# Kernel tuning notes

Hardware: AMD Instinct MI355X
Metric: run time of the kernel (lower is better)

The kernel has to match this reference:

```python
import math
import jax, jax.numpy as jnp
import numpy as np

NUM_HEADS = 16
HIDDEN = 1024
FILL = -10000000000000.0


def setup_inputs() -> dict:
    key = jax.random.key(0)
    ks = jax.random.split(key, 12)
    B, S, H = 4, 2048, HIDDEN
    scale = 1.0 / math.sqrt(H)
    inp = {
        "query": jax.random.normal(ks[0], (B, S, H), jnp.float32),
        "key": jax.random.normal(ks[1], (B, S, H), jnp.float32),
        "value": jax.random.normal(ks[2], (B, S, H), jnp.float32),
        "mask": jnp.ones((B, S), jnp.float32),
        # torch.nn.Linear weights are [out, in]; y = x @ W.T + b
        "Wq": jax.random.normal(ks[3], (H, H), jnp.float32) * scale,
        "bq": jax.random.normal(ks[4], (H,), jnp.float32) * 0.01,
        "Wk": jax.random.normal(ks[5], (H, H), jnp.float32) * scale,
        "bk": jax.random.normal(ks[6], (H,), jnp.float32) * 0.01,
        "Wv": jax.random.normal(ks[7], (H, H), jnp.float32) * scale,
        "bv": jax.random.normal(ks[8], (H,), jnp.float32) * 0.01,
        "Wo": jax.random.normal(ks[9], (H, H), jnp.float32) * scale,
        "bo": jax.random.normal(ks[10], (H,), jnp.float32) * 0.01,
    }
    return inp


def reference(query, key, value, mask, Wq, bq, Wk, bk, Wv, bv, Wo, bo):
    B, S, H = query.shape
    nh = NUM_HEADS
    dh = H // nh

    def proj(x, W, b):
        # [B,S,H] -> [B,nh,S,dh]
        y = x @ W.T + b
        return y.reshape(B, S, nh, dh).transpose(0, 2, 1, 3)

    q = proj(query, Wq, bq)
    k = proj(key, Wk, bk)
    v = proj(value, Wv, bv)

    # mask_tril=True: combined padding + causal mask [B,1,S,S]
    tril = jnp.tril(jnp.ones((S, S), query.dtype))
    m = jnp.einsum("bs,ls->bls", mask, tril)[:, None]

    scores = jnp.einsum("bhqd,bhkd->bhqk", q, k) / math.sqrt(dh)
    scores = jnp.where(m == 0, jnp.asarray(FILL, scores.dtype), scores)
    probs = jax.nn.softmax(scores, axis=-1)  # dropout p=0 -> identity

    out = jnp.einsum("bhqv,bhvd->bhqd", probs, v)
    out = out.transpose(0, 2, 1, 3).reshape(B, S, H)
    return out @ Wo.T + bo
```

## Files before the change

kernel.cpp:

```cpp
#include <hip/hip_runtime.h>
#include <hip/hip_bf16.h>
#include <math.h>

#define BATCH 4
#define SEQ   2048
#define HID   1024
#define NH    16
#define DH    64
#define MTOT  (BATCH * SEQ)
#define FILLV (-1e13f)

typedef unsigned short ushort_t;
typedef short bf16x8 __attribute__((ext_vector_type(8)));
typedef float f32x4  __attribute__((ext_vector_type(4)));

__device__ __forceinline__ float bf2f(ushort_t u) {
    return __uint_as_float(((unsigned int)u) << 16);
}
__device__ __forceinline__ ushort_t f2bf(float f) {
    union { __hip_bfloat16 h; ushort_t u; } cv;
    cv.h = __float2bfloat16(f);
    return cv.u;
}

__device__ __forceinline__ void gload16(const void* g, void* l) {
    __builtin_amdgcn_global_load_lds(
        (const __attribute__((address_space(1))) unsigned int*)g,
        (__attribute__((address_space(3))) unsigned int*)l, 16, 0, 0);
}

__global__ __launch_bounds__(256) void cast_f32_bf16(
    const float* __restrict__ x, ushort_t* __restrict__ y, int n4)
{
    const int i = blockIdx.x * 256 + threadIdx.x;
    if (i < n4) {
        const float4 v = ((const float4*)x)[i];
        ushort4 o;
        o.x = f2bf(v.x); o.y = f2bf(v.y); o.z = f2bf(v.z); o.w = f2bf(v.w);
        ((ushort4*)y)[i] = o;
    }
}

template <bool OUT_BF16, bool BIAS_ROW>
__global__ __launch_bounds__(256) void gemm_bt_mfma(
    const ushort_t* __restrict__ A,
    const ushort_t* __restrict__ W,
    const float*    __restrict__ bias,
    void* __restrict__ Yv,
    int M, int N, int K)
{
    __shared__ ushort_t As[2][4096];
    __shared__ ushort_t Bs[2][4096];

    const int tid  = threadIdx.x;
    const int lane = tid & 63;
    const int wave = tid >> 6;
    const int wm   = wave & 1;
    const int wn   = wave >> 1;

    const int flat = blockIdx.y * gridDim.x + blockIdx.x;
    const int cpx  = (gridDim.x * gridDim.y) >> 3;
    const int fl2  = (flat & 7) * cpx + (flat >> 3);
    const int bx   = fl2 % gridDim.x;
    const int by   = fl2 / gridDim.x;

    const int m0   = by * 128;
    const int n0   = bx * 128;
    const int lr   = lane & 15;
    const int lk   = (lane >> 4) * 8;

    f32x4 acc[4][4];
#pragma unroll
    for (int i = 0; i < 4; i++)
#pragma unroll
        for (int j = 0; j < 4; j++) acc[i][j] = (f32x4){0.f, 0.f, 0.f, 0.f};

    auto STAGE = [&](int kk, int d) {
        const ushort_t* a = A + (size_t)(m0 + wave * 32 + lr) * K + kk + lk;
        const ushort_t* w = W + (size_t)(n0 + wave * 32 + lr) * K + kk + lk;
        ushort_t* al = &As[d][wave * 1024];
        ushort_t* bl = &Bs[d][wave * 1024];
        gload16(a,                 al);
        gload16(a + (size_t)16 * K, al + 512);
        gload16(w,                 bl);
        gload16(w + (size_t)16 * K, bl + 512);
    };

    const int nk = K >> 5;
    STAGE(0, 0);

    for (int kt = 0; kt < nk; ++kt) {
        const int d = kt & 1;
        if (kt + 1 < nk) {
            STAGE((kt + 1) << 5, d ^ 1);
            asm volatile("s_waitcnt vmcnt(4)" ::: "memory");
        } else {
            asm volatile("s_waitcnt vmcnt(0)" ::: "memory");
        }
        __builtin_amdgcn_s_barrier();
        __builtin_amdgcn_sched_barrier(0);

        bf16x8 af[4], bf[4];
#pragma unroll
        for (int i = 0; i < 4; i++)
            af[i] = *(const bf16x8*)&As[d][(wm * 4 + i) * 512 + lane * 8];
#pragma unroll
        for (int j = 0; j < 4; j++)
            bf[j] = *(const bf16x8*)&Bs[d][(wn * 4 + j) * 512 + lane * 8];
#pragma unroll
        for (int i = 0; i < 4; i++)
#pragma unroll
            for (int j = 0; j < 4; j++)
                acc[i][j] = __builtin_amdgcn_mfma_f32_16x16x32_bf16(
                    af[i], bf[j], acc[i][j], 0, 0, 0);

        __builtin_amdgcn_sched_barrier(0);
        __builtin_amdgcn_s_barrier();
    }

    const int orow = (lane >> 4) * 4;
    const int ocol = lane & 15;

#pragma unroll
    for (int i = 0; i < 4; i++) {
#pragma unroll
        for (int j = 0; j < 4; j++) {
            const int col = n0 + wn * 64 + j * 16 + ocol;
#pragma unroll
            for (int r = 0; r < 4; r++) {
                const int row = m0 + wm * 64 + i * 16 + orow + r;
                const float bvv = BIAS_ROW ? bias[row] : bias[col];
                const float v = acc[i][j][r] + bvv;
                if (OUT_BF16)
                    ((ushort_t*)Yv)[(size_t)row * N + col] = f2bf(v);
                else
                    ((float*)Yv)[(size_t)row * N + col] = v;
            }
        }
    }
}

__global__ __launch_bounds__(256, 2) void attn_mfma(
    const ushort_t* __restrict__ Qp,
    const ushort_t* __restrict__ Kp,
    const ushort_t* __restrict__ Vt,
    const float*    __restrict__ mask,
    ushort_t* __restrict__ Op)
{
    __shared__ ushort_t Kl[2][4096];
    __shared__ ushort_t Vl[2][4096];
    __shared__ ushort_t PlA[4][16 * 72];
    __shared__ ushort_t PlB[4][16 * 72];

    const int tid  = threadIdx.x;
    const int lane = tid & 63;
    const int wave = tid >> 6;
    const int li   = lane & 15;
    const int lq   = lane >> 4;
    const int blk  = blockIdx.x;
    const int xcd = blk & 7;
    const int jj  = blk >> 3;
    const int bh  = xcd * 8 + (jj & 7);
    const int pp  = jj >> 3;
    const int pr  = pp * 4 + wave;
    const int h   = bh & (NH - 1);
    const int b   = bh >> 4;
    const int prow = lq * 4;

    const int q0a = pr * 16;
    const int q0b = (127 - pr) * 16;
    const int qrowA = q0a + li;
    const int qrowB = q0b + li;
    const int jmaxB = 31 - pp;

    const size_t bSEQ = (size_t)b * SEQ;
    const int    hoff = h * DH;

    const int srow = tid >> 3;
    const int scs8 = ((tid & 7) ^ (srow & 7)) * 8;

    const int fr0 = li * 64 + ((lq ^ (li & 7)) * 8);

    ushort_t* pwA = &PlA[wave][0];
    ushort_t* pwB = &PlB[wave][0];

    const float* mbase = mask + bSEQ + prow;

    const size_t qaA = (bSEQ + qrowA) * HID + hoff + lq * 8;
    const size_t qaB = (bSEQ + qrowB) * HID + hoff + lq * 8;
    const bf16x8 qfA0 = *(const bf16x8*)&Qp[qaA];
    const bf16x8 qfA1 = *(const bf16x8*)&Qp[qaA + 32];
    const bf16x8 qfB0 = *(const bf16x8*)&Qp[qaB];
    const bf16x8 qfB1 = *(const bf16x8*)&Qp[qaB + 32];

    f32x4 oaA[4], oaB[4];
#pragma unroll
    for (int nt = 0; nt < 4; nt++) {
        oaA[nt] = (f32x4){0.f, 0.f, 0.f, 0.f};
        oaB[nt] = (f32x4){0.f, 0.f, 0.f, 0.f};
    }
    float mA = -1e30f, lA = 0.f, mB = -1e30f, lB = 0.f;

    auto STAGE = [&](int js, int bs) {
        const size_t k0s = (size_t)js * 64;
        const ushort_t* kg = Kp + (bSEQ + k0s + srow) * HID + hoff + scs8;
        ushort_t* kl = &Kl[bs][wave * 512];
        gload16(kg, kl);
        gload16(kg + (size_t)32 * HID, kl + 2048);
        const ushort_t* vg = Vt + (size_t)(hoff + srow) * MTOT + bSEQ + k0s + scs8;
        ushort_t* vl = &Vl[bs][wave * 512];
        gload16(vg, vl);
        gload16(vg + (size_t)32 * MTOT, vl + 2048);
    };

    STAGE(0, 0);

    for (int j = 0; j <= jmaxB; ++j) {
        const int  k0  = j * 64;
        const int  bs  = j & 1;
        const bool doA = (j <= pp);

        f32x4 mk[4];
#pragma unroll
        for (int nt = 0; nt < 4; nt++)
            mk[nt] = *(const f32x4*)&mbase[k0 + nt * 16];
        __builtin_amdgcn_sched_barrier(0);

        const int jn = (j < jmaxB) ? (j + 1) : jmaxB;
        STAGE(jn, bs ^ 1);

        asm volatile("s_waitcnt vmcnt(8)" ::: "memory");
        __builtin_amdgcn_s_barrier();
        __builtin_amdgcn_sched_barrier(0);

        bf16x8 kf[4][2];
#pragma unroll
        for (int nt = 0; nt < 4; nt++) {
            const int eo = nt * 1024 + fr0;
            kf[nt][0] = *(const bf16x8*)&Kl[bs][eo];
            kf[nt][1] = *(const bf16x8*)&Kl[bs][eo ^ 32];
        }

        f32x4 saA[4], saB[4];
        __builtin_amdgcn_s_setprio(1);
#pragma unroll
        for (int nt = 0; nt < 4; nt++) {
            f32x4 a = (f32x4){0.f, 0.f, 0.f, 0.f};
            a = __builtin_amdgcn_mfma_f32_16x16x32_bf16(kf[nt][0], qfB0, a, 0, 0, 0);
            a = __builtin_amdgcn_mfma_f32_16x16x32_bf16(kf[nt][1], qfB1, a, 0, 0, 0);
            saB[nt] = a;
        }
        if (doA) {
#pragma unroll
            for (int nt = 0; nt < 4; nt++) {
                f32x4 a = (f32x4){0.f, 0.f, 0.f, 0.f};
                a = __builtin_amdgcn_mfma_f32_16x16x32_bf16(kf[nt][0], qfA0, a, 0, 0, 0);
                a = __builtin_amdgcn_mfma_f32_16x16x32_bf16(kf[nt][1], qfA1, a, 0, 0, 0);
                saA[nt] = a;
            }
        }
        __builtin_amdgcn_s_setprio(0);

        float sB[4][4];
#pragma unroll
        for (int nt = 0; nt < 4; nt++)
#pragma unroll
            for (int r = 0; r < 4; r++) {
                const float v = saB[nt][r] * 0.125f;
                sB[nt][r] = (mk[nt][r] == 0.f) ? FILLV : v;
            }
        if (k0 + 63 > q0b) {
#pragma unroll
            for (int nt = 0; nt < 4; nt++)
#pragma unroll
                for (int r = 0; r < 4; r++) {
                    const int kpos = k0 + nt * 16 + prow + r;
                    sB[nt][r] = (kpos > qrowB) ? FILLV : sB[nt][r];
                }
        }
        float pmB = fmaxf(fmaxf(sB[0][0], sB[0][1]), fmaxf(sB[0][2], sB[0][3]));
#pragma unroll
        for (int nt = 1; nt < 4; nt++)
            pmB = fmaxf(pmB, fmaxf(fmaxf(sB[nt][0], sB[nt][1]),
                                   fmaxf(sB[nt][2], sB[nt][3])));
        pmB = fmaxf(pmB, __shfl_xor(pmB, 16));
        pmB = fmaxf(pmB, __shfl_xor(pmB, 32));
        const float mnB = fmaxf(mB, pmB);
        const float alB = __expf(mB - mnB);
        mB = mnB;
        float psB = 0.f;
#pragma unroll
        for (int nt = 0; nt < 4; nt++) {
            const float p0 = __expf(sB[nt][0] - mnB);
            const float p1 = __expf(sB[nt][1] - mnB);
            const float p2 = __expf(sB[nt][2] - mnB);
            const float p3 = __expf(sB[nt][3] - mnB);
            psB += (p0 + p1) + (p2 + p3);
            ushort4 pk;
            pk.x = f2bf(p0); pk.y = f2bf(p1); pk.z = f2bf(p2); pk.w = f2bf(p3);
            *(ushort4*)&pwB[li * 72 + nt * 16 + prow] = pk;
        }
        psB += __shfl_xor(psB, 16);
        psB += __shfl_xor(psB, 32);
        lB = lB * alB + psB;

        float alA = 1.f;
        if (doA) {
            float sA[4][4];
#pragma unroll
            for (int nt = 0; nt < 4; nt++)
#pragma unroll
                for (int r = 0; r < 4; r++) {
                    const float v = saA[nt][r] * 0.125f;
                    sA[nt][r] = (mk[nt][r] == 0.f) ? FILLV : v;
                }
            if (k0 + 63 > q0a) {
#pragma unroll
                for (int nt = 0; nt < 4; nt++)
#pragma unroll
                    for (int r = 0; r < 4; r++) {
                        const int kpos = k0 + nt * 16 + prow + r;
                        sA[nt][r] = (kpos > qrowA) ? FILLV : sA[nt][r];
                    }
            }
            float pmA = fmaxf(fmaxf(sA[0][0], sA[0][1]), fmaxf(sA[0][2], sA[0][3]));
#pragma unroll
            for (int nt = 1; nt < 4; nt++)
                pmA = fmaxf(pmA, fmaxf(fmaxf(sA[nt][0], sA[nt][1]),
                                       fmaxf(sA[nt][2], sA[nt][3])));
            pmA = fmaxf(pmA, __shfl_xor(pmA, 16));
            pmA = fmaxf(pmA, __shfl_xor(pmA, 32));
            const float mnA = fmaxf(mA, pmA);
            alA = __expf(mA - mnA);
            mA = mnA;
            float psA = 0.f;
#pragma unroll
            for (int nt = 0; nt < 4; nt++) {
                const float p0 = __expf(sA[nt][0] - mnA);
                const float p1 = __expf(sA[nt][1] - mnA);
                const float p2 = __expf(sA[nt][2] - mnA);
                const float p3 = __expf(sA[nt][3] - mnA);
                psA += (p0 + p1) + (p2 + p3);
                ushort4 pk;
                pk.x = f2bf(p0); pk.y = f2bf(p1); pk.z = f2bf(p2); pk.w = f2bf(p3);
                *(ushort4*)&pwA[li * 72 + nt * 16 + prow] = pk;
            }
            psA += __shfl_xor(psA, 16);
            psA += __shfl_xor(psA, 32);
            lA = lA * alA + psA;
        }

        const bf16x8 pfB0 = *(const bf16x8*)&pwB[li * 72 + lq * 8];
        const bf16x8 pfB1 = *(const bf16x8*)&pwB[li * 72 + 32 + lq * 8];
        bf16x8 vf[4][2];
#pragma unroll
        for (int nt = 0; nt < 4; nt++) {
            const int eo = nt * 1024 + fr0;
            vf[nt][0] = *(const bf16x8*)&Vl[bs][eo];
            vf[nt][1] = *(const bf16x8*)&Vl[bs][eo ^ 32];
        }

        __builtin_amdgcn_s_setprio(1);
#pragma unroll
        for (int nt = 0; nt < 4; nt++) {
            f32x4 o = oaB[nt];
#pragma unroll
            for (int r = 0; r < 4; r++) o[r] *= alB;
            o = __builtin_amdgcn_mfma_f32_16x16x32_bf16(vf[nt][0], pfB0, o, 0, 0, 0);
            o = __builtin_amdgcn_mfma_f32_16x16x32_bf16(vf[nt][1], pfB1, o, 0, 0, 0);
            oaB[nt] = o;
        }
        __builtin_amdgcn_s_setprio(0);
        if (doA) {
            const bf16x8 pfA0 = *(const bf16x8*)&pwA[li * 72 + lq * 8];
            const bf16x8 pfA1 = *(const bf16x8*)&pwA[li * 72 + 32 + lq * 8];
            __builtin_amdgcn_s_setprio(1);
#pragma unroll
            for (int nt = 0; nt < 4; nt++) {
                f32x4 o = oaA[nt];
#pragma unroll
                for (int r = 0; r < 4; r++) o[r] *= alA;
                o = __builtin_amdgcn_mfma_f32_16x16x32_bf16(vf[nt][0], pfA0, o, 0, 0, 0);
                o = __builtin_amdgcn_mfma_f32_16x16x32_bf16(vf[nt][1], pfA1, o, 0, 0, 0);
                oaA[nt] = o;
            }
            __builtin_amdgcn_s_setprio(0);
        }

        __builtin_amdgcn_sched_barrier(0);
        __builtin_amdgcn_s_barrier();
    }
    asm volatile("s_waitcnt vmcnt(0)" ::: "memory");

    {
        const float linv = 1.f / lB;
        const size_t obase = (bSEQ + qrowB) * HID + hoff + prow;
#pragma unroll
        for (int nt = 0; nt < 4; nt++) {
            ushort4 ov;
            ov.x = f2bf(oaB[nt][0] * linv);
            ov.y = f2bf(oaB[nt][1] * linv);
            ov.z = f2bf(oaB[nt][2] * linv);
            ov.w = f2bf(oaB[nt][3] * linv);
            *(ushort4*)&Op[obase + nt * 16] = ov;
        }
    }
    {
        const float linv = 1.f / lA;
        const size_t obase = (bSEQ + qrowA) * HID + hoff + prow;
#pragma unroll
        for (int nt = 0; nt < 4; nt++) {
            ushort4 ov;
            ov.x = f2bf(oaA[nt][0] * linv);
            ov.y = f2bf(oaA[nt][1] * linv);
            ov.z = f2bf(oaA[nt][2] * linv);
            ov.w = f2bf(oaA[nt][3] * linv);
            *(ushort4*)&Op[obase + nt * 16] = ov;
        }
    }
}

extern "C" void kernel_launch(void* const* d_in, const int* in_sizes, int n_in,
                              void* d_out, int out_size, void* d_ws, size_t ws_size,
                              hipStream_t stream) {
    const float* query = (const float*)d_in[0];
    const float* key   = (const float*)d_in[1];
    const float* value = (const float*)d_in[2];
    const float* mask  = (const float*)d_in[3];
    const float* Wq    = (const float*)d_in[4];
    const float* bq    = (const float*)d_in[5];
    const float* Wk    = (const float*)d_in[6];
    const float* bk    = (const float*)d_in[7];
    const float* Wv    = (const float*)d_in[8];
    const float* bv    = (const float*)d_in[9];
    const float* Wo    = (const float*)d_in[10];
    const float* bo    = (const float*)d_in[11];

    const size_t eA = (size_t)MTOT * HID;
    const size_t eW = (size_t)HID * HID;
    ushort_t* qb  = (ushort_t*)d_ws;
    ushort_t* kb  = qb  + eA;
    ushort_t* vb  = kb  + eA;
    ushort_t* Qp  = vb  + eA;
    ushort_t* Kp  = Qp  + eA;
    ushort_t* Vtb = Kp  + eA;
    ushort_t* Op  = Vtb + eA;
    ushort_t* wqb = Op  + eA;
    ushort_t* wkb = wqb + eW;
    ushort_t* wvb = wkb + eW;
    ushort_t* wob = wvb + eW;

    const int n4a = (int)(eA / 4), n4w = (int)(eW / 4);
    cast_f32_bf16<<<(n4a + 255) / 256, 256, 0, stream>>>(query, qb, n4a);
    cast_f32_bf16<<<(n4a + 255) / 256, 256, 0, stream>>>(key,   kb, n4a);
    cast_f32_bf16<<<(n4a + 255) / 256, 256, 0, stream>>>(value, vb, n4a);
    cast_f32_bf16<<<(n4w + 255) / 256, 256, 0, stream>>>(Wq, wqb, n4w);
    cast_f32_bf16<<<(n4w + 255) / 256, 256, 0, stream>>>(Wk, wkb, n4w);
    cast_f32_bf16<<<(n4w + 255) / 256, 256, 0, stream>>>(Wv, wvb, n4w);
    cast_f32_bf16<<<(n4w + 255) / 256, 256, 0, stream>>>(Wo, wob, n4w);

    dim3 gg(HID / 128, MTOT / 128);
    gemm_bt_mfma<true, false><<<gg, 256, 0, stream>>>(qb, wqb, bq, Qp, MTOT, HID, HID);
    gemm_bt_mfma<true, false><<<gg, 256, 0, stream>>>(kb, wkb, bk, Kp, MTOT, HID, HID);
    dim3 gv(MTOT / 128, HID / 128);
    gemm_bt_mfma<true, true><<<gv, 256, 0, stream>>>(wvb, vb, bv, Vtb, HID, MTOT, HID);

    attn_mfma<<<(BATCH * NH * 64) / 4, 256, 0, stream>>>(Qp, Kp, Vtb, mask, Op);

    gemm_bt_mfma<false, false><<<gg, 256, 0, stream>>>(Op, wob, bo, d_out, MTOT, HID, HID);
}
```

Baseline: 411.9 us.

## Batch casts into two kernels and fuse Q/K/V projections into one launch

```diff
diff --git a/kernel.cpp b/kernel.cpp
--- a/kernel.cpp
+++ b/kernel.cpp
@@ -9,6 +9,8 @@
 #define DH    64
 #define MTOT  (BATCH * SEQ)
 #define FILLV (-1e13f)
+#define N4A   (MTOT * HID / 4)
+#define N4W   (HID * HID / 4)
 
 typedef unsigned short ushort_t;
 typedef short bf16x8 __attribute__((ext_vector_type(8)));
@@ -29,28 +31,56 @@
         (__attribute__((address_space(3))) unsigned int*)l, 16, 0, 0);
 }
 
-__global__ __launch_bounds__(256) void cast_f32_bf16(
-    const float* __restrict__ x, ushort_t* __restrict__ y, int n4)
+__device__ __forceinline__ ushort4 cvt4(const float4 v) {
+    ushort4 o;
+    o.x = f2bf(v.x); o.y = f2bf(v.y); o.z = f2bf(v.z); o.w = f2bf(v.w);
+    return o;
+}
+
+__global__ __launch_bounds__(256) void cast3_act(
+    const float* __restrict__ s0, const float* __restrict__ s1,
+    const float* __restrict__ s2, ushort_t* __restrict__ dst)
 {
-    const int i = blockIdx.x * 256 + threadIdx.x;
-    if (i < n4) {
-        const float4 v = ((const float4*)x)[i];
-        ushort4 o;
-        o.x = f2bf(v.x); o.y = f2bf(v.y); o.z = f2bf(v.z); o.w = f2bf(v.w);
-        ((ushort4*)y)[i] = o;
-    }
-}
-
-template <bool OUT_BF16, bool BIAS_ROW>
-__global__ __launch_bounds__(256) void gemm_bt_mfma(
-    const ushort_t* __restrict__ A,
-    const ushort_t* __restrict__ W,
-    const float*    __restrict__ bias,
-    void* __restrict__ Yv,
-    int M, int N, int K)
+    const int i   = blockIdx.x * 256 + threadIdx.x;
+    const int seg = i >> 21;
+    const int off = i & (N4A - 1);
+    const float* s = (seg == 0) ? s0 : (seg == 1) ? s1 : s2;
+    ((ushort4*)dst)[i] = cvt4(((const float4*)s)[off]);
+}
+
+__global__ __launch_bounds__(256) void cast4_w(
+    const float* __restrict__ s0, const float* __restrict__ s1,
+    const float* __restrict__ s2, const float* __restrict__ s3,
+    ushort_t* __restrict__ dst)
+{
+    const int i   = blockIdx.x * 256 + threadIdx.x;
+    const int seg = i >> 18;
+    const int off = i & (N4W - 1);
+    const float* s = (seg == 0) ? s0 : (seg == 1) ? s1 : (seg == 2) ? s2 : s3;
+    ((ushort4*)dst)[i] = cvt4(((const float4*)s)[off]);
+}
+
+__global__ __launch_bounds__(256) void qkv_gemm(
+    const ushort_t* __restrict__ A0, const ushort_t* __restrict__ A1,
+    const ushort_t* __restrict__ A2,
+    const ushort_t* __restrict__ W0, const ushort_t* __restrict__ W1,
+    const ushort_t* __restrict__ W2,
+    const float* __restrict__ b0, const float* __restrict__ b1,
+    const float* __restrict__ b2,
+    ushort_t* __restrict__ Y0, ushort_t* __restrict__ Y1,
+    ushort_t* __restrict__ Y2)
 {
     __shared__ ushort_t As[2][4096];
     __shared__ ushort_t Bs[2][4096];
+
+    const int z = blockIdx.z;
+    const ushort_t* A    = (z == 0) ? A0 : (z == 1) ? A1 : A2;
+    const ushort_t* W    = (z == 0) ? W0 : (z == 1) ? W1 : W2;
+    const float*    bias = (z == 0) ? b0 : (z == 1) ? b1 : b2;
+    ushort_t*       Y    = (z == 0) ? Y0 : (z == 1) ? Y1 : Y2;
+    const int  Nz   = (z == 2) ? MTOT : HID;
+    const int  gx   = Nz >> 7;
+    const bool brow = (z == 2);
 
     const int tid  = threadIdx.x;
     const int lane = tid & 63;
@@ -58,11 +88,10 @@
     const int wm   = wave & 1;
     const int wn   = wave >> 1;
 
-    const int flat = blockIdx.y * gridDim.x + blockIdx.x;
-    const int cpx  = (gridDim.x * gridDim.y) >> 3;
-    const int fl2  = (flat & 7) * cpx + (flat >> 3);
-    const int bx   = fl2 % gridDim.x;
-    const int by   = fl2 / gridDim.x;
+    const int flat = blockIdx.x;
+    const int fl2  = (flat & 7) * 64 + (flat >> 3);
+    const int bx   = fl2 % gx;
+    const int by   = fl2 / gx;
 
     const int m0   = by * 128;
     const int n0   = bx * 128;
@@ -76,17 +105,17 @@
         for (int j = 0; j < 4; j++) acc[i][j] = (f32x4){0.f, 0.f, 0.f, 0.f};
 
     auto STAGE = [&](int kk, int d) {
-        const ushort_t* a = A + (size_t)(m0 + wave * 32 + lr) * K + kk + lk;
-        const ushort_t* w = W + (size_t)(n0 + wave * 32 + lr) * K + kk + lk;
+        const ushort_t* a = A + (size_t)(m0 + wave * 32 + lr) * HID + kk + lk;
+        const ushort_t* w = W + (size_t)(n0 + wave * 32 + lr) * HID + kk + lk;
         ushort_t* al = &As[d][wave * 1024];
         ushort_t* bl = &Bs[d][wave * 1024];
-        gload16(a,                 al);
-        gload16(a + (size_t)16 * K, al + 512);
-        gload16(w,                 bl);
-        gload16(w + (size_t)16 * K, bl + 512);
+        gload16(a,            al);
+        gload16(a + 16 * HID, al + 512);
+        gload16(w,            bl);
+        gload16(w + 16 * HID, bl + 512);
     };
 
-    const int nk = K >> 5;
+    const int nk = HID >> 5;
     STAGE(0, 0);
 
     for (int kt = 0; kt < nk; ++kt) {
@@ -120,7 +149,6 @@
 
     const int orow = (lane >> 4) * 4;
     const int ocol = lane & 15;
-
 #pragma unroll
     for (int i = 0; i < 4; i++) {
 #pragma unroll
@@ -129,12 +157,100 @@
 #pragma unroll
             for (int r = 0; r < 4; r++) {
                 const int row = m0 + wm * 64 + i * 16 + orow + r;
-                const float bvv = BIAS_ROW ? bias[row] : bias[col];
-                const float v = acc[i][j][r] + bvv;
-                if (OUT_BF16)
-                    ((ushort_t*)Yv)[(size_t)row * N + col] = f2bf(v);
-                else
-                    ((float*)Yv)[(size_t)row * N + col] = v;
+                const float bvv = brow ? bias[row] : bias[col];
+                Y[(size_t)row * Nz + col] = f2bf(acc[i][j][r] + bvv);
+            }
+        }
+    }
+}
+
+__global__ __launch_bounds__(256) void gemm_o(
+    const ushort_t* __restrict__ A,
+    const ushort_t* __restrict__ W,
+    const float*    __restrict__ bias,
+    float* __restrict__ Yv,
+    int M, int N, int K)
+{
+    __shared__ ushort_t As[2][4096];
+    __shared__ ushort_t Bs[2][4096];
+
+    const int tid  = threadIdx.x;
+    const int lane = tid & 63;
+    const int wave = tid >> 6;
+    const int wm   = wave & 1;
+    const int wn   = wave >> 1;
+
+    const int flat = blockIdx.y * gridDim.x + blockIdx.x;
+    const int cpx  = (gridDim.x * gridDim.y) >> 3;
+    const int fl2  = (flat & 7) * cpx + (flat >> 3);
+    const int bx   = fl2 % gridDim.x;
+    const int by   = fl2 / gridDim.x;
+
+    const int m0   = by * 128;
+    const int n0   = bx * 128;
+    const int lr   = lane & 15;
+    const int lk   = (lane >> 4) * 8;
+
+    f32x4 acc[4][4];
+#pragma unroll
+    for (int i = 0; i < 4; i++)
+#pragma unroll
+        for (int j = 0; j < 4; j++) acc[i][j] = (f32x4){0.f, 0.f, 0.f, 0.f};
+
+    auto STAGE = [&](int kk, int d) {
+        const ushort_t* a = A + (size_t)(m0 + wave * 32 + lr) * K + kk + lk;
+        const ushort_t* w = W + (size_t)(n0 + wave * 32 + lr) * K + kk + lk;
+        ushort_t* al = &As[d][wave * 1024];
+        ushort_t* bl = &Bs[d][wave * 1024];
+        gload16(a,                  al);
+        gload16(a + (size_t)16 * K, al + 512);
+        gload16(w,                  bl);
+        gload16(w + (size_t)16 * K, bl + 512);
+    };
+
+    const int nk = K >> 5;
+    STAGE(0, 0);
+
+    for (int kt = 0; kt < nk; ++kt) {
+        const int d = kt & 1;
+        if (kt + 1 < nk) {
+            STAGE((kt + 1) << 5, d ^ 1);
+            asm volatile("s_waitcnt vmcnt(4)" ::: "memory");
+        } else {
+            asm volatile("s_waitcnt vmcnt(0)" ::: "memory");
+        }
+        __builtin_amdgcn_s_barrier();
+        __builtin_amdgcn_sched_barrier(0);
+
+        bf16x8 af[4], bf[4];
+#pragma unroll
+        for (int i = 0; i < 4; i++)
+            af[i] = *(const bf16x8*)&As[d][(wm * 4 + i) * 512 + lane * 8];
+#pragma unroll
+        for (int j = 0; j < 4; j++)
+            bf[j] = *(const bf16x8*)&Bs[d][(wn * 4 + j) * 512 + lane * 8];
+#pragma unroll
+        for (int i = 0; i < 4; i++)
+#pragma unroll
+            for (int j = 0; j < 4; j++)
+                acc[i][j] = __builtin_amdgcn_mfma_f32_16x16x32_bf16(
+                    af[i], bf[j], acc[i][j], 0, 0, 0);
+
+        __builtin_amdgcn_sched_barrier(0);
+        __builtin_amdgcn_s_barrier();
+    }
+
+    const int orow = (lane >> 4) * 4;
+    const int ocol = lane & 15;
+#pragma unroll
+    for (int i = 0; i < 4; i++) {
+#pragma unroll
+        for (int j = 0; j < 4; j++) {
+            const int col = n0 + wn * 64 + j * 16 + ocol;
+#pragma unroll
+            for (int r = 0; r < 4; r++) {
+                const int row = m0 + wm * 64 + i * 16 + orow + r;
+                Yv[(size_t)row * N + col] = acc[i][j][r] + bias[col];
             }
         }
     }
@@ -450,22 +566,14 @@
     ushort_t* wvb = wkb + eW;
     ushort_t* wob = wvb + eW;
 
-    const int n4a = (int)(eA / 4), n4w = (int)(eW / 4);
-    cast_f32_bf16<<<(n4a + 255) / 256, 256, 0, stream>>>(query, qb, n4a);
-    cast_f32_bf16<<<(n4a + 255) / 256, 256, 0, stream>>>(key,   kb, n4a);
-    cast_f32_bf16<<<(n4a + 255) / 256, 256, 0, stream>>>(value, vb, n4a);
-    cast_f32_bf16<<<(n4w + 255) / 256, 256, 0, stream>>>(Wq, wqb, n4w);
-    cast_f32_bf16<<<(n4w + 255) / 256, 256, 0, stream>>>(Wk, wkb, n4w);
-    cast_f32_bf16<<<(n4w + 255) / 256, 256, 0, stream>>>(Wv, wvb, n4w);
-    cast_f32_bf16<<<(n4w + 255) / 256, 256, 0, stream>>>(Wo, wob, n4w);
+    cast3_act<<<3 * N4A / 256, 256, 0, stream>>>(query, key, value, qb);
+    cast4_w  <<<4 * N4W / 256, 256, 0, stream>>>(Wq, Wk, Wv, Wo, wqb);
+
+    qkv_gemm<<<dim3(512, 1, 3), 256, 0, stream>>>(
+        qb, kb, wvb, wqb, wkb, vb, bq, bk, bv, Qp, Kp, Vtb);
+
+    attn_mfma<<<(BATCH * NH * 64) / 4, 256, 0, stream>>>(Qp, Kp, Vtb, mask, Op);
 
     dim3 gg(HID / 128, MTOT / 128);
-    gemm_bt_mfma<true, false><<<gg, 256, 0, stream>>>(qb, wqb, bq, Qp, MTOT, HID, HID);
-    gemm_bt_mfma<true, false><<<gg, 256, 0, stream>>>(kb, wkb, bk, Kp, MTOT, HID, HID);
-    dim3 gv(MTOT / 128, HID / 128);
-    gemm_bt_mfma<true, true><<<gv, 256, 0, stream>>>(wvb, vb, bv, Vtb, HID, MTOT, HID);
-
-    attn_mfma<<<(BATCH * NH * 64) / 4, 256, 0, stream>>>(Qp, Kp, Vtb, mask, Op);
-
-    gemm_bt_mfma<false, false><<<gg, 256, 0, stream>>>(Op, wob, bo, d_out, MTOT, HID, HID);
-}
+    gemm_o<<<gg, 256, 0, stream>>>(Op, wob, bo, (float*)d_out, MTOT, HID, HID);
+}
```

Measured after the change: 398.2 us. -3.3%, faster.
